# Optimization experiments

Measured on AMD Instinct MI355X. Metric: run time of the kernel, lower is better.

The kernel has to match this reference:

```python
import jax, jax.numpy as jnp
import numpy as np

_CODESZ = 8
_INT_MAP = (2 ** np.arange(_CODESZ))[::-1].astype(np.int32)  # [128,64,...,1], MSB = dim 0

_NORM12 = np.array([
    [3,1,1,1,3,3,3,3],[1,3,1,1,3,3,3,3],[1,1,3,1,3,3,3,3],[1,1,1,3,3,3,3,3],
    [3,3,3,1,3,3,1,1],[3,3,3,1,3,1,3,1],[3,3,3,1,1,3,3,1],[3,3,3,1,3,1,1,3],
    [3,3,3,1,1,3,1,3],[3,3,3,1,1,1,3,3],[3,3,1,3,3,3,1,1],[3,3,1,3,3,1,3,1],
    [3,3,1,3,1,3,3,1],[3,3,1,3,3,1,1,3],[3,3,1,3,1,3,1,3],[3,3,1,3,1,1,3,3],
    [3,1,3,3,3,3,1,1],[3,1,3,3,3,1,3,1],[3,1,3,3,1,3,3,1],[3,1,3,3,3,1,1,3],
    [3,1,3,3,1,3,1,3],[1,3,3,3,1,1,3,3],[1,3,3,3,3,3,1,1],[1,3,3,3,3,1,3,1],
    [1,3,3,3,1,3,3,1],[1,3,3,3,3,1,1,3],[1,3,3,3,1,3,1,3],[1,3,3,3,1,1,3,3],
    [3,3,1,1,3,3,3,1]], dtype=np.float32) / 2.0


def _build_codebook():
    # abs grid: nonneg half-integer vectors with norm^2 <= 10 == abs of even-sum D8+1/2 shell
    vals = np.array([0.5, 1.5, 2.5], np.float32)  # 3.5^2 > 10, so components <= 2.5
    pts = np.stack(np.meshgrid(*([vals] * _CODESZ), indexing='ij'), -1).reshape(-1, _CODESZ)
    pts = pts[(pts * pts).sum(-1) <= 10.0]                      # 227 rows
    pts = pts[np.lexsort(pts[:, ::-1].T)]                       # torch.unique(dim=0) order
    absg = np.concatenate([pts, _NORM12], 0)                    # [256, 8]

    bits = ((np.arange(256)[:, None] & _INT_MAP[None, :]) > 0).astype(np.int32)  # [256,8]
    pop = bits.sum(-1)
    even_ids = np.where(pop % 2 == 0)[0]                        # 128 even-parity masks
    odd_ids = np.where(pop % 2 == 1)[0]
    signs_even = (1 - 2 * bits[even_ids]).astype(np.float32)    # [128,8]
    signs_odd = (1 - 2 * bits[odd_ids]).astype(np.float32)
    # valid sign parity per abs entry so flipped point has even coordinate sum
    g_even = (absg.sum(-1) % 2.0) == 0.0
    S = np.where(g_even[:, None, None], signs_even[None], signs_odd[None])  # [256,128,8]
    P = (S * absg[:, None, :]).reshape(-1, _CODESZ)             # [32768,8] shell points
    # full grid = [P + 1/4 ; P - 1/4]  (grid[:half] - 1/4 == P, as the module assumes)

    # grid_part: canonical representatives (dims 1: have <=1 negative, min >= -0.5)
    sel = ((P[:, 1:] < 0).sum(-1) <= 1) & (P[:, 1:].min(-1) >= -0.5)
    grid_part = P[sel]                                          # [G,8]
    grid_part_norm = (grid_part * grid_part).sum(-1)            # [G]

    # iterate_mask: even-parity flips x grid_part -> index into grid
    flips = (1 - 2 * bits[even_ids]).astype(np.float32)         # [128,8]
    idx_map = np.zeros(256, np.int32)
    idx_map[even_ids] = np.arange(128, dtype=np.int32)
    gridH = P + 0.25                                            # first half of grid
    gridHn = (gridH * gridH).sum(-1)
    allcombo_idx = np.zeros((128, len(grid_part)), np.int32)
    for i in range(128):  # small fixed loop over sign masks, as in the original
        sc = 2.0 * ((flips[i] * grid_part) @ gridH.T) - gridHn
        allcombo_idx[i] = np.argmax(sc, -1).astype(np.int32)
    # _E8P_GRID_IDX taken as identity permutation -> grid_idx_map = arange - 2^15 (int16)
    grid_idx_map = (np.arange(2 ** 16) - 2 ** 15).astype(np.int16)
    return grid_part, grid_part_norm, allcombo_idx, idx_map, grid_idx_map


def setup_inputs() -> dict:
    key = jax.random.key(0)
    N = 131072
    grid_part, gpn, aci, imap, gim = _build_codebook()
    X = jax.random.normal(key, (N, _CODESZ), dtype=jnp.float32)
    return {
        'X': X,
        'grid_part': jnp.asarray(grid_part),
        'grid_part_norm': jnp.asarray(gpn),
        'allcombo_idx': jnp.asarray(aci),
        'idx_map': jnp.asarray(imap),
        'int_map': jnp.asarray(_INT_MAP),
        'grid_idx_map': jnp.asarray(gim),
    }


def reference(X, grid_part, grid_part_norm, allcombo_idx, idx_map, int_map, grid_idx_map):
    def fast_quantize_part(Y):
        neg = Y < 0                                              # [N,8]
        odd = (neg.sum(-1) % 2) == 1                             # [N] odd # of negatives
        Ya = jnp.abs(Y)
        Ya = Ya.at[:, 0].set(jnp.where(odd, -Ya[:, 0], Ya[:, 0]))
        mask = jnp.where(neg, -1.0, 1.0).astype(Y.dtype)
        mask = mask.at[:, 0].set(jnp.where(odd, -mask[:, 0], mask[:, 0]))
        # nearest codeword: argmax(2 Y.g - |g|^2)  == argmin |Y - g|^2
        q = jnp.argmax(2.0 * (Ya @ grid_part.T) - grid_part_norm, axis=-1)  # [N]
        vals = grid_part[q] * mask
        mint = (((1.0 - mask) * 0.5).astype(jnp.int32) * int_map).sum(-1)   # bit-pack signs
        real_idx = allcombo_idx[idx_map[mint], q]
        err = jnp.sqrt(((Y - vals) ** 2).sum(-1))
        return vals, real_idx, err

    HALF = 2 ** 15
    pv, pi, pe = fast_quantize_part(X + 0.25)
    mv, mi, me = fast_quantize_part(X - 0.25)
    which = pe < me
    final_vals = jnp.where(which[:, None], pv - 0.25, mv + 0.25)
    final_idxs = grid_idx_map[jnp.where(which, pi + HALF, mi)]
    return final_vals, final_idxs
```

## Files before the change

kernel.cpp:

```cpp
#include <hip/hip_runtime.h>
#include <hip/hip_bf16.h>

typedef __attribute__((ext_vector_type(8)))  short bf16x8;
typedef __attribute__((ext_vector_type(16))) float f32x16;

#define TPB 256
#define SCORE_MARGIN 1e-3f
#define ERR_MARGIN   1e-3f

static __device__ __forceinline__ unsigned short bf16_rne(float v) {
    union { __hip_bfloat16 h; unsigned short u; } cv;
    cv.h = __float2bfloat16(v);
    return cv.u;
}
static __device__ __forceinline__ float bfhi(unsigned u) { return __uint_as_float(u << 16); }
static __device__ __forceinline__ float bflo(unsigned u) { return __uint_as_float(u & 0xffff0000u); }

__global__ __launch_bounds__(TPB, 4) void e8p_fused(
    const float* __restrict__ X,
    const float* __restrict__ grid_part,
    const float* __restrict__ grid_part_norm,
    const int*   __restrict__ allcombo_idx,
    const int*   __restrict__ idx_map,
    float* __restrict__ out,
    int N, int G, int T)
{
    extern __shared__ __align__(16) unsigned char smem[];
    const int T32 = T * 32;
    unsigned char* ldsG = smem;
    float*         ldsNg = (float*)(smem + (size_t)T32 * 16);
    int*           ldsI  = (int*)((unsigned char*)ldsNg + (size_t)T * 32);

    __shared__ int cnt[6];
    __shared__ int cur[6];

    const int tid = threadIdx.x;

    for (int c = tid; c < T32; c += TPB) {
        uint4 z; z.x = z.y = z.z = z.w = 0u;
        *(uint4*)(ldsG + (size_t)c * 16) = z;
        ldsI[c] = -1;
    }
    for (int c = tid; c < T * 8; c += TPB) ldsNg[c] = -30000.0f;
    if (tid < 6) cnt[tid] = 0;
    if (tid >= 6 && tid < 12) cur[tid - 6] = 0;
    __syncthreads();

    for (int c = tid; c < G; c += TPB) {
        const int k = (__float2int_rn(grid_part_norm[c]) >> 1) - 1;
        atomicAdd(&cnt[k], 1);
    }
    __syncthreads();

    int offs[6];
    {
        int o = 0;
#pragma unroll
        for (int k = 0; k < 6; ++k) { offs[k] = o; o += (cnt[k] + 3) & ~3; }
    }

    for (int c = tid; c < G; c += TPB) {
        const int k = (__float2int_rn(grid_part_norm[c]) >> 1) - 1;
        const int pos = offs[k] + atomicAdd(&cur[k], 1);
        const float4 g0 = *(const float4*)(grid_part + (size_t)c * 8);
        const float4 g1 = *(const float4*)(grid_part + (size_t)c * 8 + 4);
        uint4 gv;
        gv.x = (unsigned)bf16_rne(g0.x) | ((unsigned)bf16_rne(g0.y) << 16);
        gv.y = (unsigned)bf16_rne(g0.z) | ((unsigned)bf16_rne(g0.w) << 16);
        gv.z = (unsigned)bf16_rne(g1.x) | ((unsigned)bf16_rne(g1.y) << 16);
        gv.w = (unsigned)bf16_rne(g1.z) | ((unsigned)bf16_rne(g1.w) << 16);
        *(uint4*)(ldsG + (size_t)pos * 16) = gv;
        ldsI[pos] = c;
    }
    for (int gi = tid; gi < T * 8; gi += TPB) {
        const int t = gi >> 3, hh = (gi >> 2) & 1, gg = gi & 3;
        const int p4 = t * 32 + 8 * gg + 4 * hh;
        float v = -30000.0f;
#pragma unroll
        for (int k = 0; k < 6; ++k)
            if (p4 >= offs[k] && p4 < offs[k] + cnt[k]) v = -(float)(k + 1);
        ldsNg[gi] = v;
    }
    __syncthreads();

    const int lane = tid & 63;
    const int h    = lane >> 5;
    const int col  = lane & 31;
    const int wave = blockIdx.x * (TPB / 64) + (tid >> 6);

    const int li     = col >> 1;
    const int branch = col & 1;
    const int irow   = wave * 16 + li;
    const int iload  = (irow < N) ? irow : 0;

    float x[8];
    {
        const float4 a = *(const float4*)(X + (size_t)iload * 8);
        const float4 b = *(const float4*)(X + (size_t)iload * 8 + 4);
        x[0]=a.x; x[1]=a.y; x[2]=a.z; x[3]=a.w;
        x[4]=b.x; x[5]=b.y; x[6]=b.z; x[7]=b.w;
    }

    float ya[8]; int neg = 0;
    const float sh = branch ? -0.25f : 0.25f;
#pragma unroll
    for (int j = 0; j < 8; ++j) {
        const float yj = x[j] + sh;
        if (yj < 0.0f) neg |= (1 << (7 - j));
        ya[j] = fabsf(yj);
    }
    int mint = neg;
    if (__popc(neg) & 1) { ya[0] = -ya[0]; mint ^= 128; }

    bf16x8 bfrag;
#pragma unroll
    for (int j = 0; j < 8; ++j) {
        const unsigned short hi = bf16_rne(ya[j]);
        const unsigned short lo = bf16_rne(ya[j] - bfhi((unsigned)hi));
        bfrag[j] = (short)(h ? lo : hi);
    }

    float best[4], sec[4]; int qt[4];
#pragma unroll
    for (int g = 0; g < 4; ++g) { best[g] = -1e30f; sec[g] = -1e30f; qt[g] = 0; }

    const unsigned aoff = (unsigned)col * 16u;
    const float* ngbase = ldsNg + h * 4;

    bf16x8 afragN = *(const bf16x8*)(ldsG + aoff);
    float4 ngvN   = *(const float4*)(ngbase);

    const f32x16 czero = {0,0,0,0,0,0,0,0,0,0,0,0,0,0,0,0};
    for (int t = 0; t < T; ++t) {
        const bf16x8 afrag = afragN;
        const float4 ngv   = ngvN;
        const int tn = (t + 1 < T) ? (t + 1) : t;
        afragN = *(const bf16x8*)(ldsG + (size_t)tn * 512 + aoff);
        ngvN   = *(const float4*)(ngbase + (size_t)tn * 8);

        const f32x16 acc = __builtin_amdgcn_mfma_f32_32x32x16_bf16(afrag, bfrag, czero, 0, 0, 0);
        const float ng[4] = {ngv.x, ngv.y, ngv.z, ngv.w};
#pragma unroll
        for (int g = 0; g < 4; ++g) {
            const float m = fmaxf(fmaxf(acc[4*g], acc[4*g+1]),
                                  fmaxf(acc[4*g+2], acc[4*g+3]));
            const float s = m + ng[g];
            const bool gt = s > best[g];
            sec[g]  = __builtin_amdgcn_fmed3f(s, best[g], sec[g]);
            best[g] = fmaxf(best[g], s);
            qt[g]   = gt ? t : qt[g];
        }
    }

    float bb = best[0], ss = sec[0];
    int   ib = (qt[0] << 5) + 4 * h;
#pragma unroll
    for (int g = 1; g < 4; ++g) {
        const int ibg = (qt[g] << 5) + 8 * g + 4 * h;
        const float br = best[g];
        ss = fmaxf(fmaxf(ss, sec[g]), fminf(bb, br));
        const bool take = (br > bb) || ((br == bb) && (ibg < ib));
        bb = fmaxf(bb, br);
        ib = take ? ibg : ib;
    }
    {
        const float ob = __shfl_xor(bb, 32, 64);
        const float os = __shfl_xor(ss, 32, 64);
        const int   oi = __shfl_xor(ib, 32, 64);
        ss = fmaxf(fmaxf(ss, os), fminf(bb, ob));
        const bool take = (ob > bb) || ((ob == bb) && (oi < ib));
        bb = fmaxf(bb, ob);
        ib = take ? oi : ib;
    }

    float hiF[8], loF[8];
#pragma unroll
    for (int j = 0; j < 8; ++j) {
        hiF[j] = bfhi((unsigned)bf16_rne(ya[j]));
        loF[j] = ya[j] - hiF[j];
    }
    const int tW   = ib >> 5;
    const int base = ib & 31;
    const float ngW = ldsNg[tW * 8 + ((base >> 2) & 1) * 4 + (base >> 3)];
    float sm = -1e30f, sec4 = -1e30f; int km = 0;
#pragma unroll
    for (int k = 0; k < 4; ++k) {
        const uint4 gv = *(const uint4*)(ldsG + ((size_t)tW * 32 + base + k) * 16);
        const float g0 = bfhi(gv.x), g1 = bflo(gv.x), g2 = bfhi(gv.y), g3 = bflo(gv.y);
        const float g4 = bfhi(gv.z), g5 = bflo(gv.z), g6 = bfhi(gv.w), g7 = bflo(gv.w);
        float s = ngW;
        s = fmaf(hiF[0], g0, s); s = fmaf(hiF[1], g1, s);
        s = fmaf(hiF[2], g2, s); s = fmaf(hiF[3], g3, s);
        s = fmaf(hiF[4], g4, s); s = fmaf(hiF[5], g5, s);
        s = fmaf(hiF[6], g6, s); s = fmaf(hiF[7], g7, s);
        s = fmaf(loF[0], g0, s); s = fmaf(loF[1], g1, s);
        s = fmaf(loF[2], g2, s); s = fmaf(loF[3], g3, s);
        s = fmaf(loF[4], g4, s); s = fmaf(loF[5], g5, s);
        s = fmaf(loF[6], g6, s); s = fmaf(loF[7], g7, s);
        const bool gt = s > sm;
        sec4 = __builtin_amdgcn_fmed3f(s, sm, sec4);
        sm   = fmaxf(sm, s);
        km   = gt ? k : km;
    }
    int orig = ldsI[tW * 32 + base + km];
    int closeB = ((sm - sec4) < SCORE_MARGIN) | ((bb - ss) < SCORE_MARGIN) |
                 (orig < 0);
    if (orig < 0) orig = 0;

    const int qO     = __shfl_xor(orig, 1, 64);
    const int closeO = __shfl_xor(closeB, 1, 64);
    const int mintO  = __shfl_xor(mint, 1, 64);

    const bool doEpi = (h == 0) && (branch == 0) && (irow < N);
    bool close = false;
    if (doEpi) {
        const int qP = orig, qM = qO;
        const float* gp_ = grid_part + (size_t)qP * 8;
        const float* gm_ = grid_part + (size_t)qM * 8;
        float vp[8], vm[8];
        float ep2 = 0.0f, em2 = 0.0f;
        bool coin = true;
#pragma unroll
        for (int j = 0; j < 8; ++j) {
            const float maskp = ((mint  >> (7 - j)) & 1) ? -1.0f : 1.0f;
            const float maskm = ((mintO >> (7 - j)) & 1) ? -1.0f : 1.0f;
            vp[j] = gp_[j] * maskp;
            vm[j] = gm_[j] * maskm;
            coin = coin && ((vp[j] - 0.25f) == (vm[j] + 0.25f));
            const float dpj = (x[j] + 0.25f) - vp[j];
            const float dmj = (x[j] - 0.25f) - vm[j];
            ep2 = fmaf(dpj, dpj, ep2);
            em2 = fmaf(dmj, dmj, em2);
        }
        close = closeB | closeO | (!coin && (fabsf(ep2 - em2) < ERR_MARGIN));
        if (!close) {
            const bool which = coin ? false : (ep2 < em2);
            const int rowp = idx_map[mint];
            const int rowm = idx_map[mintO];
            const int pi = allcombo_idx[(size_t)rowp * G + qP];
            const int mi = allcombo_idx[(size_t)rowm * G + qM];
            const float idxval = which ? (float)pi : (float)(mi - 32768);
            float* vout = out + (size_t)irow * 8;
#pragma unroll
            for (int j = 0; j < 8; ++j)
                vout[j] = which ? (vp[j] - 0.25f) : (vm[j] + 0.25f);
            out[(size_t)N * 8 + irow] = idxval;
        }
    }

    unsigned long long mb = __ballot(doEpi && close);
    while (mb) {
        const int b = (int)__ffsll(mb) - 1;
        mb &= (mb - 1);
        const int liF = b >> 1;
        const int iF  = wave * 16 + liF;
        float xf[8];
#pragma unroll
        for (int j = 0; j < 8; ++j) xf[j] = __shfl(x[j], b, 64);

        double yapF[8], yamF[8];
        int negp = 0, negm = 0;
#pragma unroll
        for (int j = 0; j < 8; ++j) {
            const double xd = (double)xf[j];
            const double ypd = xd + 0.25;
            const double ymd = xd - 0.25;
            if (ypd < 0.0) negp |= (1 << (7 - j));
            if (ymd < 0.0) negm |= (1 << (7 - j));
            yapF[j] = fabs(ypd);
            yamF[j] = fabs(ymd);
        }
        int mintpF = negp, mintmF = negm;
        if (__popc(negp) & 1) { yapF[0] = -yapF[0]; mintpF ^= 128; }
        if (__popc(negm) & 1) { yamF[0] = -yamF[0]; mintmF ^= 128; }

        double bestpF = -1e300, bestmF = -1e300;
        int qpF = 0x7fffffff, qmF = 0x7fffffff;
        for (int j = lane; j < G; j += 64) {
            const float4 g0 = *(const float4*)(grid_part + (size_t)j * 8);
            const float4 g1 = *(const float4*)(grid_part + (size_t)j * 8 + 4);
            const double n = (double)grid_part_norm[j];
            const double t0 = (double)g0.x, t1 = (double)g0.y,
                         t2 = (double)g0.z, t3 = (double)g0.w,
                         t4 = (double)g1.x, t5 = (double)g1.y,
                         t6 = (double)g1.z, t7 = (double)g1.w;
            double dp, dm;
            dp = yapF[0] * t0;           dm = yamF[0] * t0;
            dp = fma(yapF[1], t1, dp);   dm = fma(yamF[1], t1, dm);
            dp = fma(yapF[2], t2, dp);   dm = fma(yamF[2], t2, dm);
            dp = fma(yapF[3], t3, dp);   dm = fma(yamF[3], t3, dm);
            dp = fma(yapF[4], t4, dp);   dm = fma(yamF[4], t4, dm);
            dp = fma(yapF[5], t5, dp);   dm = fma(yamF[5], t5, dm);
            dp = fma(yapF[6], t6, dp);   dm = fma(yamF[6], t6, dm);
            dp = fma(yapF[7], t7, dp);   dm = fma(yamF[7], t7, dm);
            const double sp = 2.0 * dp - n;
            const double sm2 = 2.0 * dm - n;
            if (sp > bestpF) { bestpF = sp; qpF = j; }
            if (sm2 > bestmF) { bestmF = sm2; qmF = j; }
        }
#pragma unroll
        for (int off = 32; off > 0; off >>= 1) {
            double ob = __shfl_xor(bestpF, off, 64);
            int    oq = __shfl_xor(qpF, off, 64);
            if (ob > bestpF || (ob == bestpF && oq < qpF)) { bestpF = ob; qpF = oq; }
            ob = __shfl_xor(bestmF, off, 64);
            oq = __shfl_xor(qmF, off, 64);
            if (ob > bestmF || (ob == bestmF && oq < qmF)) { bestmF = ob; qmF = oq; }
        }
        if (lane == 0) {
            const float* gp_ = grid_part + (size_t)qpF * 8;
            const float* gm_ = grid_part + (size_t)qmF * 8;
            double vp[8], vm[8];
            double ep2 = 0.0, em2 = 0.0;
#pragma unroll
            for (int j = 0; j < 8; ++j) {
                const double maskp = ((mintpF >> (7 - j)) & 1) ? -1.0 : 1.0;
                const double maskm = ((mintmF >> (7 - j)) & 1) ? -1.0 : 1.0;
                vp[j] = (double)gp_[j] * maskp;
                vm[j] = (double)gm_[j] * maskm;
                const double xd = (double)xf[j];
                const double dpj = (xd + 0.25) - vp[j];
                const double dmj = (xd - 0.25) - vm[j];
                ep2 += dpj * dpj;
                em2 += dmj * dmj;
            }
            const double ep = sqrt(ep2), em = sqrt(em2);
            const bool which = ep < em;
            const int rowp = idx_map[mintpF];
            const int rowm = idx_map[mintmF];
            const int pi = allcombo_idx[(size_t)rowp * G + qpF];
            const int mi = allcombo_idx[(size_t)rowm * G + qmF];
            const float idxval = which ? (float)pi : (float)(mi - 32768);
            float* vout = out + (size_t)iF * 8;
#pragma unroll
            for (int j = 0; j < 8; ++j) {
                const double v = which ? (vp[j] - 0.25) : (vm[j] + 0.25);
                vout[j] = (float)v;
            }
            out[(size_t)N * 8 + iF] = idxval;
        }
    }
}

extern "C" void kernel_launch(void* const* d_in, const int* in_sizes, int n_in,
                              void* d_out, int out_size, void* d_ws, size_t ws_size,
                              hipStream_t stream) {
    const float* X    = (const float*)d_in[0];
    const float* gp   = (const float*)d_in[1];
    const float* gn   = (const float*)d_in[2];
    const int*   aci  = (const int*)d_in[3];
    const int*   imap = (const int*)d_in[4];

    const int N = in_sizes[0] / 8;
    const int G = in_sizes[1] / 8;
    const int T = (G + 18 + 31) / 32;
    const int blocks = (N + 63) / 64;
    const size_t shmem = (size_t)T * 32 * 16 + (size_t)T * 32 + (size_t)T * 32 * 4;

    hipLaunchKernelGGL(e8p_fused, dim3(blocks), dim3(TPB), shmem, stream,
                       X, gp, gn, aci, imap, (float*)d_out, N, G, T);
}
```

Baseline: 140.4 us.

## Build sorted bf16 codebook once in workspace, stream from global instead of LDS

The per-block LDS construction of the sorted bf16 codebook, norm table and index map moves into a separate single-block prep kernel that writes them to the workspace buffer. The main kernel then reads codebook fragments straight from global memory (relying on L1/L2 caching), with two-deep register prefetch instead of one. This removes the redundant per-block sort, atomics and barriers and frees LDS for occupancy. In exchange it adds a second launch, a serial one-block prep, and global-memory latency on the hot MFMA loop.

```diff
diff --git a/kernel.cpp b/kernel.cpp
--- a/kernel.cpp
+++ b/kernel.cpp
@@ -16,37 +16,32 @@
 static __device__ __forceinline__ float bfhi(unsigned u) { return __uint_as_float(u << 16); }
 static __device__ __forceinline__ float bflo(unsigned u) { return __uint_as_float(u & 0xffff0000u); }
 
-__global__ __launch_bounds__(TPB, 4) void e8p_fused(
-    const float* __restrict__ X,
+
+__global__ __launch_bounds__(256) void e8p_prep(
     const float* __restrict__ grid_part,
     const float* __restrict__ grid_part_norm,
-    const int*   __restrict__ allcombo_idx,
-    const int*   __restrict__ idx_map,
-    float* __restrict__ out,
-    int N, int G, int T)
+    unsigned char* __restrict__ ws,
+    int G, int T)
 {
-    extern __shared__ __align__(16) unsigned char smem[];
-    const int T32 = T * 32;
-    unsigned char* ldsG = smem;
-    float*         ldsNg = (float*)(smem + (size_t)T32 * 16);
-    int*           ldsI  = (int*)((unsigned char*)ldsNg + (size_t)T * 32);
-
     __shared__ int cnt[6];
     __shared__ int cur[6];
-
     const int tid = threadIdx.x;
-
-    for (int c = tid; c < T32; c += TPB) {
+    const int T32 = T * 32;
+
+    unsigned char* cwB  = ws;
+    float*         ngB  = (float*)(ws + (size_t)T32 * 16);
+    int*           rmB  = (int*)(ws + (size_t)T32 * 16 + (size_t)T * 32);
+
+    for (int c = tid; c < T32; c += 256) {
         uint4 z; z.x = z.y = z.z = z.w = 0u;
-        *(uint4*)(ldsG + (size_t)c * 16) = z;
-        ldsI[c] = -1;
-    }
-    for (int c = tid; c < T * 8; c += TPB) ldsNg[c] = -30000.0f;
-    if (tid < 6) cnt[tid] = 0;
-    if (tid >= 6 && tid < 12) cur[tid - 6] = 0;
+        *(uint4*)(cwB + (size_t)c * 16) = z;
+        rmB[c] = -1;
+    }
+    for (int c = tid; c < T * 8; c += 256) ngB[c] = -30000.0f;
+    if (tid < 6) { cnt[tid] = 0; cur[tid] = 0; }
     __syncthreads();
 
-    for (int c = tid; c < G; c += TPB) {
+    for (int c = tid; c < G; c += 256) {
         const int k = (__float2int_rn(grid_part_norm[c]) >> 1) - 1;
         atomicAdd(&cnt[k], 1);
     }
@@ -59,7 +54,7 @@
         for (int k = 0; k < 6; ++k) { offs[k] = o; o += (cnt[k] + 3) & ~3; }
     }
 
-    for (int c = tid; c < G; c += TPB) {
+    for (int c = tid; c < G; c += 256) {
         const int k = (__float2int_rn(grid_part_norm[c]) >> 1) - 1;
         const int pos = offs[k] + atomicAdd(&cur[k], 1);
         const float4 g0 = *(const float4*)(grid_part + (size_t)c * 8);
@@ -69,20 +64,38 @@
         gv.y = (unsigned)bf16_rne(g0.z) | ((unsigned)bf16_rne(g0.w) << 16);
         gv.z = (unsigned)bf16_rne(g1.x) | ((unsigned)bf16_rne(g1.y) << 16);
         gv.w = (unsigned)bf16_rne(g1.z) | ((unsigned)bf16_rne(g1.w) << 16);
-        *(uint4*)(ldsG + (size_t)pos * 16) = gv;
-        ldsI[pos] = c;
-    }
-    for (int gi = tid; gi < T * 8; gi += TPB) {
+        *(uint4*)(cwB + (size_t)pos * 16) = gv;
+        rmB[pos] = c;
+    }
+    __syncthreads();
+
+    for (int gi = tid; gi < T * 8; gi += 256) {
         const int t = gi >> 3, hh = (gi >> 2) & 1, gg = gi & 3;
         const int p4 = t * 32 + 8 * gg + 4 * hh;
         float v = -30000.0f;
 #pragma unroll
         for (int k = 0; k < 6; ++k)
             if (p4 >= offs[k] && p4 < offs[k] + cnt[k]) v = -(float)(k + 1);
-        ldsNg[gi] = v;
-    }
-    __syncthreads();
-
+        ngB[gi] = v;
+    }
+}
+
+__global__ __launch_bounds__(TPB, 4) void e8p_fused(
+    const float* __restrict__ X,
+    const float* __restrict__ grid_part,
+    const float* __restrict__ grid_part_norm,
+    const int*   __restrict__ allcombo_idx,
+    const int*   __restrict__ idx_map,
+    const unsigned char* __restrict__ ws,
+    float* __restrict__ out,
+    int N, int G, int T)
+{
+    const int T32 = T * 32;
+    const unsigned char* cwB = ws;
+    const float*         ngB = (const float*)(ws + (size_t)T32 * 16);
+    const int*           rmB = (const int*)(ws + (size_t)T32 * 16 + (size_t)T * 32);
+
+    const int tid  = threadIdx.x;
     const int lane = tid & 63;
     const int h    = lane >> 5;
     const int col  = lane & 31;
@@ -124,26 +137,29 @@
 #pragma unroll
     for (int g = 0; g < 4; ++g) { best[g] = -1e30f; sec[g] = -1e30f; qt[g] = 0; }
 
-    const unsigned aoff = (unsigned)col * 16u;
-    const float* ngbase = ldsNg + h * 4;
-
-    bf16x8 afragN = *(const bf16x8*)(ldsG + aoff);
-    float4 ngvN   = *(const float4*)(ngbase);
+    const unsigned char* aptr = cwB + (unsigned)col * 16u;
+    const float*         nptr = ngB + h * 4;
+
+    bf16x8 a0 = *(const bf16x8*)(aptr);
+    float4 n0 = *(const float4*)(nptr);
+    bf16x8 a1 = (T > 1) ? *(const bf16x8*)(aptr + 512) : a0;
+    float4 n1 = (T > 1) ? *(const float4*)(nptr + 8)   : n0;
 
     const f32x16 czero = {0,0,0,0,0,0,0,0,0,0,0,0,0,0,0,0};
     for (int t = 0; t < T; ++t) {
-        const bf16x8 afrag = afragN;
-        const float4 ngv   = ngvN;
-        const int tn = (t + 1 < T) ? (t + 1) : t;
-        afragN = *(const bf16x8*)(ldsG + (size_t)tn * 512 + aoff);
-        ngvN   = *(const float4*)(ngbase + (size_t)tn * 8);
+        const bf16x8 afrag = a0;
+        const float4 ngv   = n0;
+        a0 = a1; n0 = n1;
+        const int tn = (t + 2 < T) ? (t + 2) : t;
+        a1 = *(const bf16x8*)(aptr + (size_t)tn * 512);
+        n1 = *(const float4*)(nptr + (size_t)tn * 8);
 
         const f32x16 acc = __builtin_amdgcn_mfma_f32_32x32x16_bf16(afrag, bfrag, czero, 0, 0, 0);
         const float ng[4] = {ngv.x, ngv.y, ngv.z, ngv.w};
 #pragma unroll
         for (int g = 0; g < 4; ++g) {
-            const float m = fmaxf(fmaxf(acc[4*g], acc[4*g+1]),
-                                  fmaxf(acc[4*g+2], acc[4*g+3]));
+            const float m = fmaxf(fmaxf(fmaxf(acc[4*g], acc[4*g+1]), acc[4*g+2]),
+                                  acc[4*g+3]);
             const float s = m + ng[g];
             const bool gt = s > best[g];
             sec[g]  = __builtin_amdgcn_fmed3f(s, best[g], sec[g]);
@@ -181,11 +197,11 @@
     }
     const int tW   = ib >> 5;
     const int base = ib & 31;
-    const float ngW = ldsNg[tW * 8 + ((base >> 2) & 1) * 4 + (base >> 3)];
+    const float ngW = ngB[tW * 8 + ((base >> 2) & 1) * 4 + (base >> 3)];
     float sm = -1e30f, sec4 = -1e30f; int km = 0;
 #pragma unroll
     for (int k = 0; k < 4; ++k) {
-        const uint4 gv = *(const uint4*)(ldsG + ((size_t)tW * 32 + base + k) * 16);
+        const uint4 gv = *(const uint4*)(cwB + ((size_t)tW * 32 + base + k) * 16);
         const float g0 = bfhi(gv.x), g1 = bflo(gv.x), g2 = bfhi(gv.y), g3 = bflo(gv.y);
         const float g4 = bfhi(gv.z), g5 = bflo(gv.z), g6 = bfhi(gv.w), g7 = bflo(gv.w);
         float s = ngW;
@@ -202,9 +218,9 @@
         sm   = fmaxf(sm, s);
         km   = gt ? k : km;
     }
-    int orig = ldsI[tW * 32 + base + km];
-    int closeB = ((sm - sec4) < SCORE_MARGIN) | ((bb - ss) < SCORE_MARGIN) |
-                 (orig < 0);
+    int orig = rmB[tW * 32 + base + km];
+    const int closeB = ((sm - sec4) < SCORE_MARGIN) | ((bb - ss) < SCORE_MARGIN) |
+                       (orig < 0);
     if (orig < 0) orig = 0;
 
     const int qO     = __shfl_xor(orig, 1, 64);
@@ -355,8 +371,11 @@
     const int G = in_sizes[1] / 8;
     const int T = (G + 18 + 31) / 32;
     const int blocks = (N + 63) / 64;
-    const size_t shmem = (size_t)T * 32 * 16 + (size_t)T * 32 + (size_t)T * 32 * 4;
-
-    hipLaunchKernelGGL(e8p_fused, dim3(blocks), dim3(TPB), shmem, stream,
-                       X, gp, gn, aci, imap, (float*)d_out, N, G, T);
+
+    unsigned char* ws = (unsigned char*)d_ws;
+
+    hipLaunchKernelGGL(e8p_prep, dim3(1), dim3(256), 0, stream,
+                       gp, gn, ws, G, T);
+    hipLaunchKernelGGL(e8p_fused, dim3(blocks), dim3(TPB), 0, stream,
+                       X, gp, gn, aci, imap, ws, (float*)d_out, N, G, T);
 }
```

Result: slower. 147.2 us (+4.8%).
